# Kernel tuning notes

Hardware: AMD Instinct MI355X
Metric: run time of the kernel (lower is better)

The kernel has to match this reference:

```python
import jax, jax.numpy as jnp
import numpy as np

N_NODES = 50000
N_EDGES = 800000
NFEAT, NHID, NCLASS = 512, 128, 40
PN_SCALE = 1.0


def spmm(edge_row, edge_col, edge_val, h):
    # sparse [N,N] @ dense [N,F]: out[r] += val * h[c] for each edge (r, c)
    msgs = edge_val[:, None] * h[edge_col]  # [E, F]
    return jax.ops.segment_sum(msgs, edge_row, num_segments=N_NODES)


def pair_norm(x):
    # mode 'PN': center columns, scale by mean row norm
    x = x - x.mean(axis=0)
    rownorm_mean = jnp.sqrt(1e-6 + (x * x).sum(axis=1).mean())
    return PN_SCALE * x / rownorm_mean


def setup_inputs() -> dict:
    key = jax.random.key(0)
    ks = jax.random.split(key, 12)

    def uinit(k, shape, fan_out):
        stdv = 1.0 / np.sqrt(fan_out)
        return jax.random.uniform(k, shape, jnp.float32, -stdv, stdv)

    return {
        "x": jax.random.normal(ks[0], (N_NODES, NFEAT), jnp.float32),
        "edge_row": jax.random.randint(ks[1], (N_EDGES,), 0, N_NODES),
        "edge_col": jax.random.randint(ks[2], (N_EDGES,), 0, N_NODES),
        "edge_val": jax.random.uniform(ks[3], (N_EDGES,), jnp.float32),
        "W0": uinit(ks[4], (NFEAT, NHID), NHID),
        "b0": uinit(ks[5], (1, NHID), NHID),
        "W1": uinit(ks[6], (NHID, NHID), NHID),
        "b1": uinit(ks[7], (1, NHID), NHID),
        "W2": uinit(ks[8], (NHID, NHID), NHID),
        "b2": uinit(ks[9], (1, NHID), NHID),
        "W_out": uinit(ks[10], (NHID, NCLASS), NCLASS),
        "b_out": uinit(ks[11], (1, NCLASS), NCLASS),
    }


def reference(x, edge_row, edge_col, edge_val,
              W0, b0, W1, b1, W2, b2, W_out, b_out):
    # DeepGCN forward, eval mode (dropout p=0 is identity), residual=1 -> skip every layer
    x_old = 0.0
    for W, b in ((W0, b0), (W1, b1), (W2, b2)):
        h = x @ W                             # dense mm
        h = spmm(edge_row, edge_col, edge_val, h) + b  # sparse aggregate + bias
        h = pair_norm(h)
        h = jax.nn.relu(h)
        h = h + x_old                         # residual (x_old=0 on first layer)
        x_old = h
        x = h
    out = spmm(edge_row, edge_col, edge_val, x @ W_out) + b_out
    return out
```

## Files before the change

kernel.cpp:

```cpp
#include <hip/hip_runtime.h>
#include <hip/hip_bf16.h>
#include <math.h>

#define N_NODES 50000
#define N_EDGES 800000
#define NFEAT   512
#define NHID    128
#define NCLASS  40
#define NB_STATS 256

typedef short bf16x8 __attribute__((ext_vector_type(8)));
typedef float f32x4  __attribute__((ext_vector_type(4)));

__global__ void hist_kernel(const int* __restrict__ rows, int* __restrict__ cnt, int n) {
    int i = blockIdx.x * blockDim.x + threadIdx.x;
    if (i < n) atomicAdd(&cnt[rows[i]], 1);
}

__global__ void scan_kernel(const int* __restrict__ cnt, int* __restrict__ row_ptr,
                            int* __restrict__ cursor, int n) {
    __shared__ int wsum[16];
    __shared__ int sbase_s;
    int t = threadIdx.x;
    int lane = t & 63;
    int w = t >> 6;
    if (t == 0) { sbase_s = 0; row_ptr[0] = 0; }
    __syncthreads();
    for (int start = 0; start < n; start += 1024) {
        int i = start + t;
        int v = (i < n) ? cnt[i] : 0;
        int x = v;
        #pragma unroll
        for (int off = 1; off < 64; off <<= 1) {
            int y = __shfl_up(x, off, 64);
            if (lane >= off) x += y;
        }
        if (lane == 63) wsum[w] = x;
        __syncthreads();
        int wbase = 0;
        for (int j = 0; j < w; ++j) wbase += wsum[j];
        int sbase = sbase_s;
        int incl = sbase + wbase + x;
        if (i < n) { row_ptr[i + 1] = incl; cursor[i] = incl - v; }
        __syncthreads();
        if (t == 1023) sbase_s = incl;
        __syncthreads();
    }
}

__global__ void scatter_kernel(const int* __restrict__ rows, const int* __restrict__ cols,
                               const float* __restrict__ vals, int* __restrict__ cursor,
                               int* __restrict__ csr_col, float* __restrict__ csr_val, int n) {
    int i = blockIdx.x * blockDim.x + threadIdx.x;
    if (i < n) {
        int r = rows[i];
        int p = atomicAdd(&cursor[r], 1);
        csr_col[p] = cols[i];
        csr_val[p] = vals[i];
    }
}

__global__ __launch_bounds__(256) void wt_cvt_kernel(const float* __restrict__ W,
                                                     __hip_bfloat16* __restrict__ Wt,
                                                     int K, int N, int Nsrc) {
    int i = blockIdx.x * blockDim.x + threadIdx.x;
    if (i >= N * K) return;
    int k = i / N, n = i % N;
    float v = (n < Nsrc) ? W[k * Nsrc + n] : 0.f;
    Wt[(size_t)n * K + k] = __float2bfloat16(v);
}

template<int BM, int BN, int K>
__global__ __launch_bounds__(256) void mfma_gemm(const __hip_bfloat16* __restrict__ Xb,
                                                 const __hip_bfloat16* __restrict__ Wt,
                                                 __hip_bfloat16* __restrict__ Ob, int M) {
    constexpr int BK  = 64;
    constexpr int LDK = 72;
    constexpr int WN  = BN / 64;
    __shared__ short As[BM * LDK];
    __shared__ short Bs[BN * LDK];
    int t = threadIdx.x;
    int lane = t & 63;
    int w = t >> 6;
    int wm = w / WN, wn = w % WN;
    int row0 = blockIdx.x * BM;
    int m0 = wm * 32, n0 = wn * 64;
    int l15 = lane & 15, quad = lane >> 4;

    f32x4 acc[2][4] = {};

    for (int k0 = 0; k0 < K; k0 += BK) {
        #pragma unroll
        for (int idx = t; idx < BM * 8; idx += 256) {
            int r = idx >> 3, c = idx & 7;
            uint4 v = make_uint4(0u, 0u, 0u, 0u);
            if (row0 + r < M)
                v = *(const uint4*)(Xb + (size_t)(row0 + r) * K + k0 + c * 8);
            *(uint4*)(As + r * LDK + c * 8) = v;
        }
        #pragma unroll
        for (int idx = t; idx < BN * 8; idx += 256) {
            int r = idx >> 3, c = idx & 7;
            uint4 v = *(const uint4*)(Wt + (size_t)r * K + k0 + c * 8);
            *(uint4*)(Bs + r * LDK + c * 8) = v;
        }
        __syncthreads();
        #pragma unroll
        for (int ks = 0; ks < 2; ++ks) {
            bf16x8 af[2], bfv[4];
            #pragma unroll
            for (int mt = 0; mt < 2; ++mt)
                af[mt] = *(const bf16x8*)(As + (m0 + mt * 16 + l15) * LDK + ks * 32 + quad * 8);
            #pragma unroll
            for (int nt = 0; nt < 4; ++nt)
                bfv[nt] = *(const bf16x8*)(Bs + (n0 + nt * 16 + l15) * LDK + ks * 32 + quad * 8);
            #pragma unroll
            for (int mt = 0; mt < 2; ++mt)
                #pragma unroll
                for (int nt = 0; nt < 4; ++nt)
                    acc[mt][nt] = __builtin_amdgcn_mfma_f32_16x16x32_bf16(
                        af[mt], bfv[nt], acc[mt][nt], 0, 0, 0);
        }
        __syncthreads();
    }
    #pragma unroll
    for (int mt = 0; mt < 2; ++mt) {
        #pragma unroll
        for (int reg = 0; reg < 4; ++reg) {
            int row = row0 + m0 + mt * 16 + quad * 4 + reg;
            if (row < M) {
                #pragma unroll
                for (int nt = 0; nt < 4; ++nt)
                    Ob[(size_t)row * BN + n0 + nt * 16 + l15] =
                        __float2bfloat16(acc[mt][nt][reg]);
            }
        }
    }
}

template<int BM, int BN, int K>
__global__ __launch_bounds__(256) void mfma_gemm_f32a(const float* __restrict__ Xg,
                                                      const __hip_bfloat16* __restrict__ Wt,
                                                      __hip_bfloat16* __restrict__ Ob, int M) {
    constexpr int BK  = 64;
    constexpr int LDK = 72;
    constexpr int WN  = BN / 64;
    __shared__ short As[BM * LDK];
    __shared__ short Bs[BN * LDK];
    int t = threadIdx.x;
    int lane = t & 63;
    int w = t >> 6;
    int wm = w / WN, wn = w % WN;
    int row0 = blockIdx.x * BM;
    int m0 = wm * 32, n0 = wn * 64;
    int l15 = lane & 15, quad = lane >> 4;

    f32x4 acc[2][4] = {};

    for (int k0 = 0; k0 < K; k0 += BK) {
        #pragma unroll
        for (int idx = t; idx < BM * 16; idx += 256) {
            int r = idx >> 4, c = idx & 15;
            float4 v = make_float4(0.f, 0.f, 0.f, 0.f);
            if (row0 + r < M)
                v = *(const float4*)(Xg + (size_t)(row0 + r) * K + k0 + c * 4);
            __hip_bfloat16 o[4] = {__float2bfloat16(v.x), __float2bfloat16(v.y),
                                   __float2bfloat16(v.z), __float2bfloat16(v.w)};
            *(short4*)(As + r * LDK + c * 4) = *(short4*)o;
        }
        #pragma unroll
        for (int idx = t; idx < BN * 8; idx += 256) {
            int r = idx >> 3, c = idx & 7;
            uint4 v = *(const uint4*)(Wt + (size_t)r * K + k0 + c * 8);
            *(uint4*)(Bs + r * LDK + c * 8) = v;
        }
        __syncthreads();
        #pragma unroll
        for (int ks = 0; ks < 2; ++ks) {
            bf16x8 af[2], bfv[4];
            #pragma unroll
            for (int mt = 0; mt < 2; ++mt)
                af[mt] = *(const bf16x8*)(As + (m0 + mt * 16 + l15) * LDK + ks * 32 + quad * 8);
            #pragma unroll
            for (int nt = 0; nt < 4; ++nt)
                bfv[nt] = *(const bf16x8*)(Bs + (n0 + nt * 16 + l15) * LDK + ks * 32 + quad * 8);
            #pragma unroll
            for (int mt = 0; mt < 2; ++mt)
                #pragma unroll
                for (int nt = 0; nt < 4; ++nt)
                    acc[mt][nt] = __builtin_amdgcn_mfma_f32_16x16x32_bf16(
                        af[mt], bfv[nt], acc[mt][nt], 0, 0, 0);
        }
        __syncthreads();
    }
    #pragma unroll
    for (int mt = 0; mt < 2; ++mt) {
        #pragma unroll
        for (int reg = 0; reg < 4; ++reg) {
            int row = row0 + m0 + mt * 16 + quad * 4 + reg;
            if (row < M) {
                #pragma unroll
                for (int nt = 0; nt < 4; ++nt)
                    Ob[(size_t)row * BN + n0 + nt * 16 + l15] =
                        __float2bfloat16(acc[mt][nt][reg]);
            }
        }
    }
}

__global__ __launch_bounds__(256) void spmm_bf16_kernel(const __hip_bfloat16* __restrict__ H,
                                                        const int* __restrict__ row_ptr,
                                                        const int* __restrict__ cols,
                                                        const float* __restrict__ vals,
                                                        const float* __restrict__ bias,
                                                        __hip_bfloat16* __restrict__ Bm,
                                                        int nrows) {
    int wid = (int)((blockIdx.x * blockDim.x + threadIdx.x) >> 6);
    wid = __builtin_amdgcn_readfirstlane(wid);
    int lane = threadIdx.x & 63;
    if (wid >= nrows) return;
    int s = row_ptr[wid];
    int e = row_ptr[wid + 1];
    float2 bv = *(const float2*)(bias + 2 * lane);
    float acc0 = bv.x, acc1 = bv.y;
    const __hip_bfloat162* H2 = (const __hip_bfloat162*)H;
    int i = s;
    for (; i + 3 < e; i += 4) {
        int   c0 = cols[i],     c1 = cols[i + 1], c2 = cols[i + 2], c3 = cols[i + 3];
        float v0 = vals[i],     v1 = vals[i + 1], v2 = vals[i + 2], v3 = vals[i + 3];
        __hip_bfloat162 h0 = H2[(size_t)c0 * 64 + lane];
        __hip_bfloat162 h1 = H2[(size_t)c1 * 64 + lane];
        __hip_bfloat162 h2 = H2[(size_t)c2 * 64 + lane];
        __hip_bfloat162 h3 = H2[(size_t)c3 * 64 + lane];
        acc0 = fmaf(v0, __bfloat162float(h0.x), acc0); acc1 = fmaf(v0, __bfloat162float(h0.y), acc1);
        acc0 = fmaf(v1, __bfloat162float(h1.x), acc0); acc1 = fmaf(v1, __bfloat162float(h1.y), acc1);
        acc0 = fmaf(v2, __bfloat162float(h2.x), acc0); acc1 = fmaf(v2, __bfloat162float(h2.y), acc1);
        acc0 = fmaf(v3, __bfloat162float(h3.x), acc0); acc1 = fmaf(v3, __bfloat162float(h3.y), acc1);
    }
    for (; i < e; ++i) {
        int c = cols[i]; float v = vals[i];
        __hip_bfloat162 h = H2[(size_t)c * 64 + lane];
        acc0 = fmaf(v, __bfloat162float(h.x), acc0);
        acc1 = fmaf(v, __bfloat162float(h.y), acc1);
    }
    __hip_bfloat16 o[2] = {__float2bfloat16(acc0), __float2bfloat16(acc1)};
    *(ushort2*)(Bm + (size_t)wid * 128 + 2 * lane) = *(ushort2*)o;
}

__global__ __launch_bounds__(256) void stats_kernel(const __hip_bfloat16* __restrict__ B,
                                                    float* __restrict__ partials, int n2) {
    int tid = blockIdx.x * blockDim.x + threadIdx.x;
    int stride = NB_STATS * 256;
    const __hip_bfloat162* B2 = (const __hip_bfloat162*)B;
    float cs0 = 0.f, cs1 = 0.f, sq = 0.f;
    for (int j = tid; j < n2; j += stride) {
        __hip_bfloat162 h = B2[j];
        float a = __bfloat162float(h.x), b = __bfloat162float(h.y);
        cs0 += a; cs1 += b;
        sq = fmaf(a, a, sq); sq = fmaf(b, b, sq);
    }
    __shared__ float s0[256], s1[256], ss[256];
    int t = threadIdx.x;
    s0[t] = cs0; s1[t] = cs1; ss[t] = sq;
    __syncthreads();
    if (t < 64) {
        float a = s0[t] + s0[t + 64] + s0[t + 128] + s0[t + 192];
        float b = s1[t] + s1[t + 64] + s1[t + 128] + s1[t + 192];
        float* pb = partials + (size_t)blockIdx.x * 132;
        pb[2 * t] = a;
        pb[2 * t + 1] = b;
    }
    __syncthreads();
    for (int off = 128; off > 0; off >>= 1) {
        if (t < off) ss[t] += ss[t + off];
        __syncthreads();
    }
    if (t == 0) partials[(size_t)blockIdx.x * 132 + 128] = ss[0];
}

__global__ void finalize_stats_kernel(const float* __restrict__ partials,
                                      float* __restrict__ stats, int nrows) {
    int t = threadIdx.x;
    float cs = 0.f;
    for (int b = 0; b < NB_STATS; ++b) cs += partials[(size_t)b * 132 + t];
    float mu = cs / (float)nrows;
    __shared__ float smu2[128];
    __shared__ float ssq[128];
    float sq = 0.f;
    for (int b = t; b < NB_STATS; b += 128) sq += partials[(size_t)b * 132 + 128];
    smu2[t] = mu * mu;
    ssq[t] = sq;
    __syncthreads();
    for (int off = 64; off > 0; off >>= 1) {
        if (t < off) { smu2[t] += smu2[t + off]; ssq[t] += ssq[t + off]; }
        __syncthreads();
    }
    if (t == 0) {
        float ms = ssq[0] / (float)nrows - smu2[0];
        stats[129] = 1.0f / sqrtf(1e-6f + ms);
    }
    stats[t] = mu;
}

__global__ __launch_bounds__(256) void pn_apply_kernel(const __hip_bfloat16* __restrict__ B,
                                                       const float* __restrict__ stats,
                                                       __hip_bfloat16* __restrict__ Xb,
                                                       int n4, int addResid) {
    int i = blockIdx.x * blockDim.x + threadIdx.x;
    if (i >= n4) return;
    ushort4 bv = *(const ushort4*)(B + (size_t)i * 4);
    __hip_bfloat16* bb = (__hip_bfloat16*)&bv;
    int c4 = (i << 2) & 127;
    float s = stats[129];
    float4 m = ((const float4*)stats)[c4 >> 2];
    float r0 = 0.f, r1 = 0.f, r2 = 0.f, r3 = 0.f;
    if (addResid) {
        ushort4 rv = *(const ushort4*)(Xb + (size_t)i * 4);
        __hip_bfloat16* rb = (__hip_bfloat16*)&rv;
        r0 = __bfloat162float(rb[0]); r1 = __bfloat162float(rb[1]);
        r2 = __bfloat162float(rb[2]); r3 = __bfloat162float(rb[3]);
    }
    __hip_bfloat16 o[4];
    o[0] = __float2bfloat16(fmaxf((__bfloat162float(bb[0]) - m.x) * s, 0.f) + r0);
    o[1] = __float2bfloat16(fmaxf((__bfloat162float(bb[1]) - m.y) * s, 0.f) + r1);
    o[2] = __float2bfloat16(fmaxf((__bfloat162float(bb[2]) - m.z) * s, 0.f) + r2);
    o[3] = __float2bfloat16(fmaxf((__bfloat162float(bb[3]) - m.w) * s, 0.f) + r3);
    *(ushort4*)(Xb + (size_t)i * 4) = *(ushort4*)o;
}

__global__ __launch_bounds__(256) void spmm_out_kernel(const __hip_bfloat16* __restrict__ G,
                                                       const int* __restrict__ row_ptr,
                                                       const int* __restrict__ cols,
                                                       const float* __restrict__ vals,
                                                       const float* __restrict__ bias,
                                                       float* __restrict__ out, int nrows) {
    int wid = (int)((blockIdx.x * blockDim.x + threadIdx.x) >> 6);
    wid = __builtin_amdgcn_readfirstlane(wid);
    int lane = threadIdx.x & 63;
    if (wid >= nrows) return;
    int s = row_ptr[wid];
    int e = row_ptr[wid + 1];
    float acc = (lane < NCLASS) ? bias[lane] : 0.f;
    int i = s;
    for (; i + 3 < e; i += 4) {
        int   c0 = cols[i],     c1 = cols[i + 1], c2 = cols[i + 2], c3 = cols[i + 3];
        float v0 = vals[i],     v1 = vals[i + 1], v2 = vals[i + 2], v3 = vals[i + 3];
        float g0 = __bfloat162float(G[(size_t)c0 * 64 + lane]);
        float g1 = __bfloat162float(G[(size_t)c1 * 64 + lane]);
        float g2 = __bfloat162float(G[(size_t)c2 * 64 + lane]);
        float g3 = __bfloat162float(G[(size_t)c3 * 64 + lane]);
        acc = fmaf(v0, g0, acc); acc = fmaf(v1, g1, acc);
        acc = fmaf(v2, g2, acc); acc = fmaf(v3, g3, acc);
    }
    for (; i < e; ++i)
        acc = fmaf(vals[i], __bfloat162float(G[(size_t)cols[i] * 64 + lane]), acc);
    if (lane < NCLASS) out[(size_t)wid * NCLASS + lane] = acc;
}

extern "C" void kernel_launch(void* const* d_in, const int* in_sizes, int n_in,
                              void* d_out, int out_size, void* d_ws, size_t ws_size,
                              hipStream_t stream) {
    const float* x        = (const float*)d_in[0];
    const int*   edge_row = (const int*)  d_in[1];
    const int*   edge_col = (const int*)  d_in[2];
    const float* edge_val = (const float*)d_in[3];
    const float* W0 = (const float*)d_in[4];
    const float* b0 = (const float*)d_in[5];
    const float* W1 = (const float*)d_in[6];
    const float* b1 = (const float*)d_in[7];
    const float* W2 = (const float*)d_in[8];
    const float* b2 = (const float*)d_in[9];
    const float* W_out = (const float*)d_in[10];
    const float* b_out = (const float*)d_in[11];
    float* out = (float*)d_out;

    const size_t NH = (size_t)N_NODES * NHID;

    char* p = (char*)d_ws;
    __hip_bfloat16* Xb   = (__hip_bfloat16*)p;  p += NH * 2;
    __hip_bfloat16* A_bf = (__hip_bfloat16*)p;  p += NH * 2;
    __hip_bfloat16* Bm   = (__hip_bfloat16*)p;  p += NH * 2;
    __hip_bfloat16* Wt0 = (__hip_bfloat16*)p;   p += (size_t)128 * 512 * 2;
    __hip_bfloat16* Wt1 = (__hip_bfloat16*)p;   p += (size_t)128 * 128 * 2;
    __hip_bfloat16* Wt2 = (__hip_bfloat16*)p;   p += (size_t)128 * 128 * 2;
    __hip_bfloat16* Wot = (__hip_bfloat16*)p;   p += (size_t)64 * 128 * 2;
    float* stats    = (float*)p;                p += 132 * 4;
    float* partials = (float*)p;                p += (size_t)NB_STATS * 132 * 4;
    int* cnt      = (int*)p;                    p += (size_t)N_NODES * 4;
    int* row_ptr  = (int*)p;                    p += (size_t)(N_NODES + 1) * 4;
    int* cursor   = (int*)p;                    p += (size_t)N_NODES * 4;
    int* csr_col  = (int*)p;                    p += (size_t)N_EDGES * 4;
    float* csr_val = (float*)p;

    const int EB = N_EDGES / 256;
    const int SPMM_GRID = (N_NODES + 3) / 4;
    const int PN_GRID = (int)(NH / 4 + 255) / 256;

    wt_cvt_kernel<<<(512 * 128 + 255) / 256, 256, 0, stream>>>(W0, Wt0, 512, 128, 128);
    wt_cvt_kernel<<<(128 * 128 + 255) / 256, 256, 0, stream>>>(W1, Wt1, 128, 128, 128);
    wt_cvt_kernel<<<(128 * 128 + 255) / 256, 256, 0, stream>>>(W2, Wt2, 128, 128, 128);
    wt_cvt_kernel<<<(128 * 64 + 255) / 256, 256, 0, stream>>>(W_out, Wot, 128, 64, 40);

    hipMemsetAsync(cnt, 0, N_NODES * sizeof(int), stream);
    hist_kernel<<<EB, 256, 0, stream>>>(edge_row, cnt, N_EDGES);
    scan_kernel<<<1, 1024, 0, stream>>>(cnt, row_ptr, cursor, N_NODES);
    scatter_kernel<<<EB, 256, 0, stream>>>(edge_row, edge_col, edge_val, cursor,
                                           csr_col, csr_val, N_EDGES);

    mfma_gemm_f32a<64, 128, 512><<<(N_NODES + 63) / 64, 256, 0, stream>>>(x, Wt0, A_bf, N_NODES);
    spmm_bf16_kernel<<<SPMM_GRID, 256, 0, stream>>>(A_bf, row_ptr, csr_col, csr_val, b0, Bm, N_NODES);
    stats_kernel<<<NB_STATS, 256, 0, stream>>>(Bm, partials, (int)(NH / 2));
    finalize_stats_kernel<<<1, 128, 0, stream>>>(partials, stats, N_NODES);
    pn_apply_kernel<<<PN_GRID, 256, 0, stream>>>(Bm, stats, Xb, (int)(NH / 4), 0);

    const __hip_bfloat16* Wts[2] = {Wt1, Wt2};
    const float* bs[2] = {b1, b2};
    for (int l = 0; l < 2; ++l) {
        mfma_gemm<64, 128, 128><<<(N_NODES + 63) / 64, 256, 0, stream>>>(Xb, Wts[l], A_bf, N_NODES);
        spmm_bf16_kernel<<<SPMM_GRID, 256, 0, stream>>>(A_bf, row_ptr, csr_col, csr_val, bs[l], Bm, N_NODES);
        stats_kernel<<<NB_STATS, 256, 0, stream>>>(Bm, partials, (int)(NH / 2));
        finalize_stats_kernel<<<1, 128, 0, stream>>>(partials, stats, N_NODES);
        pn_apply_kernel<<<PN_GRID, 256, 0, stream>>>(Bm, stats, Xb, (int)(NH / 4), 1);
    }

    mfma_gemm<128, 64, 128><<<(N_NODES + 127) / 128, 256, 0, stream>>>(Xb, Wot, A_bf, N_NODES);
    spmm_out_kernel<<<SPMM_GRID, 256, 0, stream>>>(A_bf, row_ptr, csr_col, csr_val, b_out,
                                                   out, N_NODES);
}
```

Baseline: 571.3 us.

## Interleave CSR col/val, split SpMM lanes across edges, parallelize scan and scatter

The separate CSR column and value arrays are packed into one int2 array, and each wave in the SpMM kernels now handles two edges at once, one per half-wave, using wider gathers. The partial sums are then combined with a cross-lane shuffle. The scan is restructured so each thread scans its own chunk instead of looping serially over 1024-wide blocks. The scatter runs in row-range passes to improve locality of the atomic writes. The four weight-conversion launches are merged into one. Together these aim to cut gather latency and setup overhead, at the cost of extra scatter blocks that each re-read the edge list.

```diff
diff --git a/kernel.cpp b/kernel.cpp
--- a/kernel.cpp
+++ b/kernel.cpp
@@ -8,9 +8,15 @@
 #define NHID    128
 #define NCLASS  40
 #define NB_STATS 256
+#define NPASS    8
+#define ROWS_PER_PASS (N_NODES / NPASS)
 
 typedef short bf16x8 __attribute__((ext_vector_type(8)));
 typedef float f32x4  __attribute__((ext_vector_type(4)));
+
+__device__ inline float bf2f(unsigned short u) {
+    union { unsigned int i; float f; } x; x.i = ((unsigned int)u) << 16; return x.f;
+}
 
 __global__ void hist_kernel(const int* __restrict__ rows, int* __restrict__ cnt, int n) {
     int i = blockIdx.x * blockDim.x + threadIdx.x;
@@ -19,55 +25,68 @@
 
 __global__ void scan_kernel(const int* __restrict__ cnt, int* __restrict__ row_ptr,
                             int* __restrict__ cursor, int n) {
+    const int CH = (n + 1023) / 1024;
     __shared__ int wsum[16];
-    __shared__ int sbase_s;
     int t = threadIdx.x;
-    int lane = t & 63;
-    int w = t >> 6;
-    if (t == 0) { sbase_s = 0; row_ptr[0] = 0; }
+    int lane = t & 63, w = t >> 6;
+    int start = t * CH;
+    int end = min(start + CH, n);
+    int sum = 0;
+    for (int i = start; i < end; ++i) sum += cnt[i];
+    int x = sum;
+    #pragma unroll
+    for (int off = 1; off < 64; off <<= 1) {
+        int y = __shfl_up(x, off, 64);
+        if (lane >= off) x += y;
+    }
+    if (lane == 63) wsum[w] = x;
     __syncthreads();
-    for (int start = 0; start < n; start += 1024) {
-        int i = start + t;
-        int v = (i < n) ? cnt[i] : 0;
-        int x = v;
-        #pragma unroll
-        for (int off = 1; off < 64; off <<= 1) {
-            int y = __shfl_up(x, off, 64);
-            if (lane >= off) x += y;
-        }
-        if (lane == 63) wsum[w] = x;
-        __syncthreads();
-        int wbase = 0;
-        for (int j = 0; j < w; ++j) wbase += wsum[j];
-        int sbase = sbase_s;
-        int incl = sbase + wbase + x;
-        if (i < n) { row_ptr[i + 1] = incl; cursor[i] = incl - v; }
-        __syncthreads();
-        if (t == 1023) sbase_s = incl;
-        __syncthreads();
+    int wbase = 0;
+    for (int j = 0; j < w; ++j) wbase += wsum[j];
+    int run = wbase + (x - sum);
+    if (t == 0) row_ptr[0] = 0;
+    for (int i = start; i < end; ++i) {
+        int c = cnt[i];
+        cursor[i] = run;
+        run += c;
+        row_ptr[i + 1] = run;
     }
 }
 
 __global__ void scatter_kernel(const int* __restrict__ rows, const int* __restrict__ cols,
                                const float* __restrict__ vals, int* __restrict__ cursor,
-                               int* __restrict__ csr_col, float* __restrict__ csr_val, int n) {
+                               int2* __restrict__ csr_cv, int n, int blocksPerPass) {
+    int p = blockIdx.x / blocksPerPass;
+    int b = blockIdx.x % blocksPerPass;
+    int i = b * 256 + threadIdx.x;
+    if (i >= n) return;
+    int r = rows[i];
+    int lo = p * ROWS_PER_PASS;
+    if (r < lo || r >= lo + ROWS_PER_PASS) return;
+    int pos = atomicAdd(&cursor[r], 1);
+    csr_cv[pos] = make_int2(cols[i], __float_as_int(vals[i]));
+}
+
+__global__ __launch_bounds__(256) void wt_cvt_all_kernel(const float* __restrict__ W0,
+        const float* __restrict__ W1, const float* __restrict__ W2,
+        const float* __restrict__ Wo, __hip_bfloat16* __restrict__ Wt0,
+        __hip_bfloat16* __restrict__ Wt1, __hip_bfloat16* __restrict__ Wt2,
+        __hip_bfloat16* __restrict__ Wot) {
     int i = blockIdx.x * blockDim.x + threadIdx.x;
-    if (i < n) {
-        int r = rows[i];
-        int p = atomicAdd(&cursor[r], 1);
-        csr_col[p] = cols[i];
-        csr_val[p] = vals[i];
-    }
-}
-
-__global__ __launch_bounds__(256) void wt_cvt_kernel(const float* __restrict__ W,
-                                                     __hip_bfloat16* __restrict__ Wt,
-                                                     int K, int N, int Nsrc) {
-    int i = blockIdx.x * blockDim.x + threadIdx.x;
-    if (i >= N * K) return;
-    int k = i / N, n = i % N;
-    float v = (n < Nsrc) ? W[k * Nsrc + n] : 0.f;
-    Wt[(size_t)n * K + k] = __float2bfloat16(v);
+    if (i < 65536) {
+        int k = i >> 7, n = i & 127;
+        Wt0[(size_t)n * 512 + k] = __float2bfloat16(W0[i]);
+    } else if (i < 65536 + 16384) {
+        int j = i - 65536; int k = j >> 7, n = j & 127;
+        Wt1[(size_t)n * 128 + k] = __float2bfloat16(W1[j]);
+    } else if (i < 65536 + 32768) {
+        int j = i - 65536 - 16384; int k = j >> 7, n = j & 127;
+        Wt2[(size_t)n * 128 + k] = __float2bfloat16(W2[j]);
+    } else if (i < 65536 + 32768 + 8192) {
+        int j = i - 65536 - 32768; int k = j >> 6, n = j & 63;
+        float v = (n < NCLASS) ? Wo[k * NCLASS + n] : 0.f;
+        Wot[(size_t)n * 128 + k] = __float2bfloat16(v);
+    }
 }
 
 template<int BM, int BN, int K>
@@ -210,41 +229,51 @@
 
 __global__ __launch_bounds__(256) void spmm_bf16_kernel(const __hip_bfloat16* __restrict__ H,
                                                         const int* __restrict__ row_ptr,
-                                                        const int* __restrict__ cols,
-                                                        const float* __restrict__ vals,
+                                                        const int2* __restrict__ cv,
                                                         const float* __restrict__ bias,
                                                         __hip_bfloat16* __restrict__ Bm,
                                                         int nrows) {
     int wid = (int)((blockIdx.x * blockDim.x + threadIdx.x) >> 6);
     wid = __builtin_amdgcn_readfirstlane(wid);
     int lane = threadIdx.x & 63;
+    int h = lane >> 5;
+    int sub = lane & 31;
     if (wid >= nrows) return;
     int s = row_ptr[wid];
     int e = row_ptr[wid + 1];
-    float2 bv = *(const float2*)(bias + 2 * lane);
-    float acc0 = bv.x, acc1 = bv.y;
-    const __hip_bfloat162* H2 = (const __hip_bfloat162*)H;
+    const ushort4* H4 = (const ushort4*)H;
+    f32x4 acc = {0.f, 0.f, 0.f, 0.f};
     int i = s;
     for (; i + 3 < e; i += 4) {
-        int   c0 = cols[i],     c1 = cols[i + 1], c2 = cols[i + 2], c3 = cols[i + 3];
-        float v0 = vals[i],     v1 = vals[i + 1], v2 = vals[i + 2], v3 = vals[i + 3];
-        __hip_bfloat162 h0 = H2[(size_t)c0 * 64 + lane];
-        __hip_bfloat162 h1 = H2[(size_t)c1 * 64 + lane];
-        __hip_bfloat162 h2 = H2[(size_t)c2 * 64 + lane];
-        __hip_bfloat162 h3 = H2[(size_t)c3 * 64 + lane];
-        acc0 = fmaf(v0, __bfloat162float(h0.x), acc0); acc1 = fmaf(v0, __bfloat162float(h0.y), acc1);
-        acc0 = fmaf(v1, __bfloat162float(h1.x), acc0); acc1 = fmaf(v1, __bfloat162float(h1.y), acc1);
-        acc0 = fmaf(v2, __bfloat162float(h2.x), acc0); acc1 = fmaf(v2, __bfloat162float(h2.y), acc1);
-        acc0 = fmaf(v3, __bfloat162float(h3.x), acc0); acc1 = fmaf(v3, __bfloat162float(h3.y), acc1);
+        int2 c0 = cv[i], c1 = cv[i + 1], c2 = cv[i + 2], c3 = cv[i + 3];
+        int   ca = h ? c2.x : c0.x;
+        float va = __int_as_float(h ? c2.y : c0.y);
+        int   cb = h ? c3.x : c1.x;
+        float vb = __int_as_float(h ? c3.y : c1.y);
+        ushort4 ga = H4[(size_t)ca * 32 + sub];
+        ushort4 gb = H4[(size_t)cb * 32 + sub];
+        acc[0] = fmaf(va, bf2f(ga.x), acc[0]); acc[1] = fmaf(va, bf2f(ga.y), acc[1]);
+        acc[2] = fmaf(va, bf2f(ga.z), acc[2]); acc[3] = fmaf(va, bf2f(ga.w), acc[3]);
+        acc[0] = fmaf(vb, bf2f(gb.x), acc[0]); acc[1] = fmaf(vb, bf2f(gb.y), acc[1]);
+        acc[2] = fmaf(vb, bf2f(gb.z), acc[2]); acc[3] = fmaf(vb, bf2f(gb.w), acc[3]);
     }
     for (; i < e; ++i) {
-        int c = cols[i]; float v = vals[i];
-        __hip_bfloat162 h = H2[(size_t)c * 64 + lane];
-        acc0 = fmaf(v, __bfloat162float(h.x), acc0);
-        acc1 = fmaf(v, __bfloat162float(h.y), acc1);
-    }
-    __hip_bfloat16 o[2] = {__float2bfloat16(acc0), __float2bfloat16(acc1)};
-    *(ushort2*)(Bm + (size_t)wid * 128 + 2 * lane) = *(ushort2*)o;
+        int2 c = cv[i];
+        if (h == 0) {
+            float v = __int_as_float(c.y);
+            ushort4 g = H4[(size_t)c.x * 32 + sub];
+            acc[0] = fmaf(v, bf2f(g.x), acc[0]); acc[1] = fmaf(v, bf2f(g.y), acc[1]);
+            acc[2] = fmaf(v, bf2f(g.z), acc[2]); acc[3] = fmaf(v, bf2f(g.w), acc[3]);
+        }
+    }
+    #pragma unroll
+    for (int c = 0; c < 4; ++c) acc[c] += __shfl_xor(acc[c], 32);
+    if (h == 0) {
+        float4 b4 = *(const float4*)(bias + 4 * sub);
+        __hip_bfloat16 o[4] = {__float2bfloat16(acc[0] + b4.x), __float2bfloat16(acc[1] + b4.y),
+                               __float2bfloat16(acc[2] + b4.z), __float2bfloat16(acc[3] + b4.w)};
+        *(ushort4*)(Bm + (size_t)wid * 128 + 4 * sub) = *(ushort4*)o;
+    }
 }
 
 __global__ __launch_bounds__(256) void stats_kernel(const __hip_bfloat16* __restrict__ B,
@@ -330,31 +359,47 @@
 
 __global__ __launch_bounds__(256) void spmm_out_kernel(const __hip_bfloat16* __restrict__ G,
                                                        const int* __restrict__ row_ptr,
-                                                       const int* __restrict__ cols,
-                                                       const float* __restrict__ vals,
+                                                       const int2* __restrict__ cv,
                                                        const float* __restrict__ bias,
                                                        float* __restrict__ out, int nrows) {
     int wid = (int)((blockIdx.x * blockDim.x + threadIdx.x) >> 6);
     wid = __builtin_amdgcn_readfirstlane(wid);
     int lane = threadIdx.x & 63;
+    int h = lane >> 5;
+    int sub = lane & 31;
     if (wid >= nrows) return;
     int s = row_ptr[wid];
     int e = row_ptr[wid + 1];
-    float acc = (lane < NCLASS) ? bias[lane] : 0.f;
+    const __hip_bfloat162* G2 = (const __hip_bfloat162*)G;
+    float a0 = 0.f, a1 = 0.f;
     int i = s;
     for (; i + 3 < e; i += 4) {
-        int   c0 = cols[i],     c1 = cols[i + 1], c2 = cols[i + 2], c3 = cols[i + 3];
-        float v0 = vals[i],     v1 = vals[i + 1], v2 = vals[i + 2], v3 = vals[i + 3];
-        float g0 = __bfloat162float(G[(size_t)c0 * 64 + lane]);
-        float g1 = __bfloat162float(G[(size_t)c1 * 64 + lane]);
-        float g2 = __bfloat162float(G[(size_t)c2 * 64 + lane]);
-        float g3 = __bfloat162float(G[(size_t)c3 * 64 + lane]);
-        acc = fmaf(v0, g0, acc); acc = fmaf(v1, g1, acc);
-        acc = fmaf(v2, g2, acc); acc = fmaf(v3, g3, acc);
-    }
-    for (; i < e; ++i)
-        acc = fmaf(vals[i], __bfloat162float(G[(size_t)cols[i] * 64 + lane]), acc);
-    if (lane < NCLASS) out[(size_t)wid * NCLASS + lane] = acc;
+        int2 c0 = cv[i], c1 = cv[i + 1], c2 = cv[i + 2], c3 = cv[i + 3];
+        int   ca = h ? c2.x : c0.x;
+        float va = __int_as_float(h ? c2.y : c0.y);
+        int   cb = h ? c3.x : c1.x;
+        float vb = __int_as_float(h ? c3.y : c1.y);
+        __hip_bfloat162 ga = G2[(size_t)ca * 32 + sub];
+        __hip_bfloat162 gb = G2[(size_t)cb * 32 + sub];
+        a0 = fmaf(va, __bfloat162float(ga.x), a0); a1 = fmaf(va, __bfloat162float(ga.y), a1);
+        a0 = fmaf(vb, __bfloat162float(gb.x), a0); a1 = fmaf(vb, __bfloat162float(gb.y), a1);
+    }
+    for (; i < e; ++i) {
+        int2 c = cv[i];
+        if (h == 0) {
+            float v = __int_as_float(c.y);
+            __hip_bfloat162 g = G2[(size_t)c.x * 32 + sub];
+            a0 = fmaf(v, __bfloat162float(g.x), a0);
+            a1 = fmaf(v, __bfloat162float(g.y), a1);
+        }
+    }
+    a0 += __shfl_xor(a0, 32);
+    a1 += __shfl_xor(a1, 32);
+    if (h == 0 && sub < NCLASS / 2) {
+        float2 b2 = *(const float2*)(bias + 2 * sub);
+        float2 o = make_float2(a0 + b2.x, a1 + b2.y);
+        *(float2*)(out + (size_t)wid * NCLASS + 2 * sub) = o;
+    }
 }
 
 extern "C" void kernel_launch(void* const* d_in, const int* in_sizes, int n_in,
@@ -387,28 +432,25 @@
     float* stats    = (float*)p;                p += 132 * 4;
     float* partials = (float*)p;                p += (size_t)NB_STATS * 132 * 4;
     int* cnt      = (int*)p;                    p += (size_t)N_NODES * 4;
-    int* row_ptr  = (int*)p;                    p += (size_t)(N_NODES + 1) * 4;
+    int* row_ptr  = (int*)p;                    p += (size_t)(N_NODES + 1) * 4 + 4;
     int* cursor   = (int*)p;                    p += (size_t)N_NODES * 4;
-    int* csr_col  = (int*)p;                    p += (size_t)N_EDGES * 4;
-    float* csr_val = (float*)p;
-
-    const int EB = N_EDGES / 256;
+    int2* csr_cv  = (int2*)p;                   p += (size_t)N_EDGES * 8;
+
+    const int EB = (N_EDGES + 255) / 256;
     const int SPMM_GRID = (N_NODES + 3) / 4;
     const int PN_GRID = (int)(NH / 4 + 255) / 256;
 
-    wt_cvt_kernel<<<(512 * 128 + 255) / 256, 256, 0, stream>>>(W0, Wt0, 512, 128, 128);
-    wt_cvt_kernel<<<(128 * 128 + 255) / 256, 256, 0, stream>>>(W1, Wt1, 128, 128, 128);
-    wt_cvt_kernel<<<(128 * 128 + 255) / 256, 256, 0, stream>>>(W2, Wt2, 128, 128, 128);
-    wt_cvt_kernel<<<(128 * 64 + 255) / 256, 256, 0, stream>>>(W_out, Wot, 128, 64, 40);
+    wt_cvt_all_kernel<<<(65536 + 32768 + 8192 + 255) / 256, 256, 0, stream>>>(
+        W0, W1, W2, W_out, Wt0, Wt1, Wt2, Wot);
 
     hipMemsetAsync(cnt, 0, N_NODES * sizeof(int), stream);
     hist_kernel<<<EB, 256, 0, stream>>>(edge_row, cnt, N_EDGES);
     scan_kernel<<<1, 1024, 0, stream>>>(cnt, row_ptr, cursor, N_NODES);
-    scatter_kernel<<<EB, 256, 0, stream>>>(edge_row, edge_col, edge_val, cursor,
-                                           csr_col, csr_val, N_EDGES);
+    scatter_kernel<<<EB * NPASS, 256, 0, stream>>>(edge_row, edge_col, edge_val, cursor,
+                                                   csr_cv, N_EDGES, EB);
 
     mfma_gemm_f32a<64, 128, 512><<<(N_NODES + 63) / 64, 256, 0, stream>>>(x, Wt0, A_bf, N_NODES);
-    spmm_bf16_kernel<<<SPMM_GRID, 256, 0, stream>>>(A_bf, row_ptr, csr_col, csr_val, b0, Bm, N_NODES);
+    spmm_bf16_kernel<<<SPMM_GRID, 256, 0, stream>>>(A_bf, row_ptr, csr_cv, b0, Bm, N_NODES);
     stats_kernel<<<NB_STATS, 256, 0, stream>>>(Bm, partials, (int)(NH / 2));
     finalize_stats_kernel<<<1, 128, 0, stream>>>(partials, stats, N_NODES);
     pn_apply_kernel<<<PN_GRID, 256, 0, stream>>>(Bm, stats, Xb, (int)(NH / 4), 0);
@@ -417,13 +459,13 @@
     const float* bs[2] = {b1, b2};
     for (int l = 0; l < 2; ++l) {
         mfma_gemm<64, 128, 128><<<(N_NODES + 63) / 64, 256, 0, stream>>>(Xb, Wts[l], A_bf, N_NODES);
-        spmm_bf16_kernel<<<SPMM_GRID, 256, 0, stream>>>(A_bf, row_ptr, csr_col, csr_val, bs[l], Bm, N_NODES);
+        spmm_bf16_kernel<<<SPMM_GRID, 256, 0, stream>>>(A_bf, row_ptr, csr_cv, bs[l], Bm, N_NODES);
         stats_kernel<<<NB_STATS, 256, 0, stream>>>(Bm, partials, (int)(NH / 2));
         finalize_stats_kernel<<<1, 128, 0, stream>>>(partials, stats, N_NODES);
         pn_apply_kernel<<<PN_GRID, 256, 0, stream>>>(Bm, stats, Xb, (int)(NH / 4), 1);
     }
 
     mfma_gemm<128, 64, 128><<<(N_NODES + 127) / 128, 256, 0, stream>>>(Xb, Wot, A_bf, N_NODES);
-    spmm_out_kernel<<<SPMM_GRID, 256, 0, stream>>>(A_bf, row_ptr, csr_col, csr_val, b_out,
+    spmm_out_kernel<<<SPMM_GRID, 256, 0, stream>>>(A_bf, row_ptr, csr_cv, b_out,
                                                    out, N_NODES);
 }
```

New measurement: 616.3 us. 1.08x slower.
